# Kernel optimization log

Hardware: AMD Instinct MI355X
Metric: run time of the kernel (lower is better)

The kernel has to match this reference:

```python
import jax, jax.numpy as jnp
import numpy as np

NS, NV = 32, 8                      # scalar / vector multiplicities (32x0e + 8x1o)
N_NODES, N_EDGES = 16384, 131072
NEF, HID = 128, 128                 # edge feature dim, MLP hidden
WN = NS*NS + NV*NS + NS*NV + NV*NV  # 1600 tensor-product weights per edge
D = NS + 3*NV                       # 56 node feature dim
INV_SQRT3 = 1.0/np.sqrt(3.0)        # CG coeff for 1o x 1o -> 0e
PATH_NORM = 1.0/np.sqrt(NS + NV)    # fan-in normalization per output irrep
EPS = 1e-5


def setup_inputs() -> dict:
    key = jax.random.key(0)
    ks = jax.random.split(key, 10)
    node_attr = jax.random.normal(ks[0], (N_NODES, D), jnp.float32)
    edge_index = jax.random.randint(ks[1], (2, N_EDGES), 0, N_NODES, dtype=jnp.int64)
    edge_attr = jax.random.normal(ks[2], (N_EDGES, NEF), jnp.float32)
    edge_sh = jax.random.normal(ks[3], (N_EDGES, 4), jnp.float32)
    W1 = jax.random.normal(ks[4], (NEF, HID), jnp.float32) / np.sqrt(NEF)
    b1 = jnp.zeros((HID,), jnp.float32)
    W2 = jax.random.normal(ks[5], (HID, WN), jnp.float32) / np.sqrt(HID)
    b2 = jnp.zeros((WN,), jnp.float32)
    bn_gamma = jnp.ones((NS + NV,), jnp.float32)   # per-irrep scale (scalars then vectors)
    bn_beta = jnp.zeros((NS,), jnp.float32)        # bias only on scalar irreps
    return dict(node_attr=node_attr, edge_attr=edge_attr, edge_sh=edge_sh,
                W1=W1, b1=b1, W2=W2, b2=b2, bn_gamma=bn_gamma, bn_beta=bn_beta,
                edge_index=edge_index)


def reference(node_attr, edge_attr, edge_sh, W1, b1, W2, b2, bn_gamma, bn_beta, edge_index):
    edge_src, edge_dst = edge_index[0], edge_index[1]

    # per-edge tensor-product weights from edge MLP (dropout=0, eval mode)
    w = jax.nn.relu(edge_attr @ W1 + b1) @ W2 + b2            # [E, WN]
    o0 = NS*NS; o1 = o0 + NV*NS; o2 = o1 + NS*NV
    w_ss = w[:, :o0].reshape(-1, NS, NS)   # 0e x 0e -> 0e
    w_vs = w[:, o0:o1].reshape(-1, NV, NS) # 1o x 1o -> 0e
    w_sv = w[:, o1:o2].reshape(-1, NS, NV) # 0e x 1o -> 1o
    w_vv = w[:, o2:].reshape(-1, NV, NV)   # 1o x 0e -> 1o

    # gather node features onto edges
    x = node_attr[edge_dst]                # [E, D]
    xs = x[:, :NS]                         # [E, NS]
    xv = x[:, NS:].reshape(-1, NV, 3)      # [E, NV, 3]
    ss = edge_sh[:, 0]                     # [E]
    sv = edge_sh[:, 1:4]                   # [E, 3]

    # CG tensor product with per-edge fully-connected weights
    dot_vv = jnp.einsum('eim,em->ei', xv, sv) * INV_SQRT3
    out_s = (jnp.einsum('eij,ei->ej', w_ss, xs) * ss[:, None]
             + jnp.einsum('eij,ei->ej', w_vs, dot_vv)) * PATH_NORM          # [E, NS]
    out_v = (jnp.einsum('eij,ei->ej', w_sv, xs)[:, :, None] * sv[:, None, :]
             + jnp.einsum('eij,eim->ejm', w_vv, xv) * ss[:, None, None]) * PATH_NORM  # [E, NV, 3]
    tp = jnp.concatenate([out_s, out_v.reshape(-1, 3*NV)], axis=-1)         # [E, D]

    # scatter-mean to source nodes
    sums = jax.ops.segment_sum(tp, edge_src, num_segments=N_NODES)
    cnt = jax.ops.segment_sum(jnp.ones((tp.shape[0], 1), tp.dtype), edge_src,
                              num_segments=N_NODES)
    out = sums / jnp.maximum(cnt, 1.0)

    # residual (in/out irreps identical -> zero padding is a no-op)
    out = out + node_attr

    # equivariant batch norm (training-mode batch statistics)
    s = out[:, :NS]
    v = out[:, NS:].reshape(-1, NV, 3)
    s = (s - s.mean(0)) / jnp.sqrt(s.var(0) + EPS) * bn_gamma[:NS] + bn_beta
    vn2 = (v * v).sum(-1).mean(0)                               # [NV] mean squared norm
    v = v / jnp.sqrt(vn2 + EPS)[None, :, None] * bn_gamma[NS:][None, :, None]
    return jnp.concatenate([s, v.reshape(-1, 3*NV)], axis=-1)
```

## Files before the change

### kernel.cpp

```cpp
#include <hip/hip_runtime.h>

typedef short short8 __attribute__((ext_vector_type(8)));
typedef unsigned short us4 __attribute__((ext_vector_type(4)));
typedef float floatx4 __attribute__((ext_vector_type(4)));
typedef unsigned short u16;

#define NN 16384
#define NE 131072
#define NEF_ 128
#define DD 56
#define INV_SQRT3F 0.57735026918962576f
#define PATH_NORMF 0.15811388300841897f

__device__ __forceinline__ float bf2f(u16 u) {
    union { unsigned int i; float f; } v; v.i = ((unsigned int)u) << 16; return v.f;
}
__device__ __forceinline__ u16 f2bf(float f) {
    union { float f; unsigned int i; } v; v.f = f;
    unsigned int r = v.i + 0x7fffu + ((v.i >> 16) & 1u);
    return (u16)(r >> 16);
}

__global__ __launch_bounds__(256) void prep(const float* __restrict__ W1,
                                            const float* __restrict__ W2,
                                            u16* __restrict__ W1f,
                                            u16* __restrict__ W2f,
                                            const int* __restrict__ eidx,
                                            int* __restrict__ deg) {
    int b = blockIdx.x;
    if (b < 864) {
        int i = b * 256 + threadIdx.x;
        if (i < 16384) {
            int cc = i >> 13, kk = (i >> 11) & 3, cg = (i >> 9) & 3;
            int lane = (i >> 3) & 63, j = i & 7;
            int q = lane >> 4, m = lane & 15;
            W1f[i] = f2bf(W1[(kk * 32 + q * 8 + j) * 128 + cc * 64 + cg * 16 + m]);
        } else {
            int f = i - 16384;
            int c = f >> 13, kk = (f >> 11) & 3, cg = (f >> 9) & 3;
            int lane = (f >> 3) & 63, j = f & 7;
            int q = lane >> 4, m = lane & 15;
            W2f[f] = f2bf(W2[(kk * 32 + q * 8 + j) * 1600 + c * 64 + cg * 16 + m]);
        }
    } else {
        int e = (b - 864) * 256 + threadIdx.x;
        atomicAdd(&deg[eidx[e]], 1);
    }
}

__global__ __launch_bounds__(1024) void deg_scan(const int* __restrict__ deg,
                                                 int* __restrict__ row_start,
                                                 int* __restrict__ cursor) {
    __shared__ int part[1024];
    const int t = threadIdx.x;
    const int base = t * 16;
    int loc[16];
    int s = 0;
    #pragma unroll
    for (int i = 0; i < 16; i++) { loc[i] = s; s += deg[base + i]; }
    part[t] = s;
    __syncthreads();
    for (int off = 1; off < 1024; off <<= 1) {
        int v = (t >= off) ? part[t - off] : 0;
        __syncthreads();
        part[t] += v;
        __syncthreads();
    }
    int pre = (t == 0) ? 0 : part[t - 1];
    #pragma unroll
    for (int i = 0; i < 16; i++) {
        int v = pre + loc[i];
        row_start[base + i] = v;
        cursor[base + i] = v;
    }
    if (t == 1023) row_start[16384] = pre + s;
}

__global__ __launch_bounds__(256) void edge_scatter(const int* __restrict__ eidx,
                                                    int* __restrict__ cursor,
                                                    int* __restrict__ edge_order) {
    int e = blockIdx.x * 256 + threadIdx.x;
    int p = atomicAdd(&cursor[eidx[e]], 1);
    edge_order[p] = e;
}

__global__ __launch_bounds__(512, 4) void tpconv(
    const float* __restrict__ node_attr, const float* __restrict__ edge_attr,
    const float* __restrict__ edge_sh, const u16* __restrict__ W1f,
    const float* __restrict__ b1, const u16* __restrict__ W2f,
    const float* __restrict__ b2, const int* __restrict__ eidx,
    const int* __restrict__ edge_order,
    float* __restrict__ tp)
{
    __shared__ __align__(16) char smem[48896];
    u16*   sA  = (u16*)smem;
    u16*   B2a = (u16*)(smem + 17408);
    u16*   B2b = (u16*)smem;
    u16*   sF  = (u16*)(smem + 33792);
    float* b2s = (float*)(smem + 42496);
    float* Ssc  = (float*)smem;
    float* Svec = (float*)(smem + 16896);

    const int t = threadIdx.x;
    const int lane = t & 63;
    const int wv = t >> 6;
    const int m = lane & 15;
    const int q = lane >> 4;
    const int cg = wv & 3;
    const int eh = wv >> 2;
    const int eb = eh * 32;
    const int p0 = blockIdx.x * 64;

    short8 pre[2];
    #pragma unroll
    for (int ii = 0; ii < 2; ii++)
        pre[ii] = *(const short8*)&W2f[ii * 4096 + t * 8];

    for (int i = t; i < 1600; i += 512) b2s[i] = b2[i];

    #pragma unroll
    for (int ii = 0; ii < 4; ii++) {
        int cid = t + 512 * ii;
        int r = cid >> 5, s = cid & 31;
        int e = edge_order[p0 + r];
        const float* src = &edge_attr[(size_t)e * NEF_ + s * 4];
        us4 o;
        o.x = f2bf(src[0]); o.y = f2bf(src[1]); o.z = f2bf(src[2]); o.w = f2bf(src[3]);
        *(us4*)&sA[r * 136 + s * 4] = o;
    }
    if (t < 64) {
        int e = edge_order[p0 + t];
        int nd = eidx[NE + e];
        const float* na = node_attr + (size_t)nd * DD;
        const float* sh = edge_sh + (size_t)e * 4;
        float ss = sh[0], s0 = sh[1], s1 = sh[2], s2 = sh[3];
        #pragma unroll
        for (int i = 0; i < 32; i++) sF[i * 64 + t] = f2bf(na[i]);
        #pragma unroll
        for (int i = 0; i < 8; i++) {
            float d = (na[32+i*3]*s0 + na[33+i*3]*s1 + na[34+i*3]*s2) * INV_SQRT3F;
            sF[(32 + i) * 64 + t] = f2bf(d);
        }
        #pragma unroll
        for (int i = 0; i < 24; i++) sF[(40 + i) * 64 + t] = f2bf(na[32 + i]);
        sF[64 * 64 + t] = f2bf(ss);
        sF[65 * 64 + t] = f2bf(s0);
        sF[66 * 64 + t] = f2bf(s1);
        sF[67 * 64 + t] = f2bf(s2);
    }
    __syncthreads();

    floatx4 hacc[2][2];
    #pragma unroll
    for (int cc = 0; cc < 2; cc++) {
        #pragma unroll
        for (int ii = 0; ii < 2; ii++)
            *(short8*)&B2a[ii * 4096 + t * 8] =
                *(const short8*)&W1f[cc * 8192 + ii * 4096 + t * 8];
        __syncthreads();
        {
            float bv = b1[cc * 64 + cg * 16 + m];
            hacc[cc][0] = (floatx4){bv, bv, bv, bv};
            hacc[cc][1] = hacc[cc][0];
        }
        #pragma unroll
        for (int kk = 0; kk < 4; kk++) {
            short8 a0 = *(const short8*)&sA[(eb      + m) * 136 + kk * 32 + q * 8];
            short8 a1 = *(const short8*)&sA[(eb + 16 + m) * 136 + kk * 32 + q * 8];
            short8 bA = *(const short8*)&B2a[(kk * 4 + cg) * 512 + lane * 8];
            hacc[cc][0] = __builtin_amdgcn_mfma_f32_16x16x32_bf16(a0, bA, hacc[cc][0], 0, 0, 0);
            hacc[cc][1] = __builtin_amdgcn_mfma_f32_16x16x32_bf16(a1, bA, hacc[cc][1], 0, 0, 0);
        }
        __syncthreads();
    }
    #pragma unroll
    for (int cc = 0; cc < 2; cc++)
      #pragma unroll
      for (int rt = 0; rt < 2; rt++)
        #pragma unroll
        for (int r = 0; r < 4; r++) {
            int e   = eb + rt * 16 + q * 4 + r;
            int col = cc * 64 + cg * 16 + m;
            float v = hacc[cc][rt][r];
            sA[e * 136 + col] = f2bf(v > 0.f ? v : 0.f);
        }
    __syncthreads();

    short8 hc[2][4];
    #pragma unroll
    for (int et = 0; et < 2; et++)
        #pragma unroll
        for (int kk = 0; kk < 4; kk++)
            hc[et][kk] = *(const short8*)&sA[(eb + et * 16 + m) * 136 + kk * 32 + q * 8];

    float ssc[2], svc[2][3];
    #pragma unroll
    for (int et = 0; et < 2; et++) {
        ssc[et] = bf2f(sF[64 * 64 + eb + et * 16 + m]);
        svc[et][0] = bf2f(sF[65 * 64 + eb + et * 16 + m]);
        svc[et][1] = bf2f(sF[66 * 64 + eb + et * 16 + m]);
        svc[et][2] = bf2f(sF[67 * 64 + eb + et * 16 + m]);
    }

    #pragma unroll
    for (int ii = 0; ii < 2; ii++)
        *(short8*)&B2a[ii * 4096 + t * 8] = pre[ii];
    #pragma unroll
    for (int ii = 0; ii < 2; ii++)
        pre[ii] = *(const short8*)&W2f[8192 + ii * 4096 + t * 8];
    __syncthreads();

    float tps[2][4];
    float tpv[2][4][3];
    #pragma unroll
    for (int et = 0; et < 2; et++)
        #pragma unroll
        for (int r = 0; r < 4; r++) {
            tps[et][r] = 0.f;
            tpv[et][r][0] = 0.f; tpv[et][r][1] = 0.f; tpv[et][r][2] = 0.f;
        }

    for (int c = 0; c < 25; c++) {
        const u16* rb = (c & 1) ? B2b : B2a;
        u16*       wb = (c & 1) ? B2a : B2b;

        floatx4 bias = *(const floatx4*)&b2s[c * 64 + cg * 16 + q * 4];
        floatx4 acc[2];
        acc[0] = bias; acc[1] = bias;
        #pragma unroll
        for (int kk = 0; kk < 4; kk++) {
            short8 a = *(const short8*)&rb[(kk * 4 + cg) * 512 + lane * 8];
            acc[0] = __builtin_amdgcn_mfma_f32_16x16x32_bf16(a, hc[0][kk], acc[0], 0, 0, 0);
            acc[1] = __builtin_amdgcn_mfma_f32_16x16x32_bf16(a, hc[1][kk], acc[1], 0, 0, 0);
        }

        if (c < 24) {
            #pragma unroll
            for (int ii = 0; ii < 2; ii++)
                *(short8*)&wb[ii * 4096 + t * 8] = pre[ii];
            if (c < 23) {
                #pragma unroll
                for (int ii = 0; ii < 2; ii++)
                    pre[ii] = *(const short8*)&W2f[(size_t)(c + 2) * 8192 + ii * 4096 + t * 8];
            }
        }

        if (c < 16) {
            const int i = 2 * c + (cg >> 1);
            #pragma unroll
            for (int et = 0; et < 2; et++) {
                float f = bf2f(sF[i * 64 + eb + et * 16 + m]) * ssc[et];
                #pragma unroll
                for (int r = 0; r < 4; r++) tps[et][r] += acc[et][r] * f;
            }
        } else if (c < 20) {
            const int i = 2 * (c - 16) + (cg >> 1);
            #pragma unroll
            for (int et = 0; et < 2; et++) {
                float f = bf2f(sF[(32 + i) * 64 + eb + et * 16 + m]);
                #pragma unroll
                for (int r = 0; r < 4; r++) tps[et][r] += acc[et][r] * f;
            }
        } else if (c < 24) {
            const int i = 8 * (c - 20) + cg * 2 + (q >> 1);
            #pragma unroll
            for (int et = 0; et < 2; et++) {
                float f = bf2f(sF[i * 64 + eb + et * 16 + m]);
                #pragma unroll
                for (int r = 0; r < 4; r++) {
                    float t0 = acc[et][r] * f;
                    tpv[et][r][0] += t0 * svc[et][0];
                    tpv[et][r][1] += t0 * svc[et][1];
                    tpv[et][r][2] += t0 * svc[et][2];
                }
            }
        } else {
            const int i = cg * 2 + (q >> 1);
            #pragma unroll
            for (int et = 0; et < 2; et++) {
                float x0 = bf2f(sF[(40 + 3 * i + 0) * 64 + eb + et * 16 + m]) * ssc[et];
                float x1 = bf2f(sF[(40 + 3 * i + 1) * 64 + eb + et * 16 + m]) * ssc[et];
                float x2 = bf2f(sF[(40 + 3 * i + 2) * 64 + eb + et * 16 + m]) * ssc[et];
                #pragma unroll
                for (int r = 0; r < 4; r++) {
                    tpv[et][r][0] += acc[et][r] * x0;
                    tpv[et][r][1] += acc[et][r] * x1;
                    tpv[et][r][2] += acc[et][r] * x2;
                }
            }
        }

        __syncthreads();
    }

    #pragma unroll
    for (int et = 0; et < 2; et++)
        #pragma unroll
        for (int r = 0; r < 4; r++)
            Ssc[(cg >> 1) * 2112 + (eb + et * 16 + m) * 33 + (cg & 1) * 16 + q * 4 + r] = tps[et][r];
    #pragma unroll
    for (int et = 0; et < 2; et++)
        #pragma unroll
        for (int r = 0; r < 4; r++)
            #pragma unroll
            for (int mm = 0; mm < 3; mm++) {
                float v = tpv[et][r][mm];
                v += __shfl_xor(v, 32, 64);
                if (q < 2)
                    Svec[cg * 1600 + (eb + et * 16 + m) * 25 + ((q & 1) * 4 + r) * 3 + mm] = v;
            }
    __syncthreads();

    for (int idx = t; idx < 3584; idx += 512) {
        int e = idx / 56, d = idx - e * 56;
        float v;
        if (d < 32) {
            v = Ssc[e * 33 + d] + Ssc[2112 + e * 33 + d];
        } else {
            int dd = d - 32;
            v = Svec[e * 25 + dd] + Svec[1600 + e * 25 + dd]
              + Svec[3200 + e * 25 + dd] + Svec[4800 + e * 25 + dd];
        }
        tp[(size_t)(p0 + e) * DD + d] = v * PATH_NORMF;
    }
}

__global__ __launch_bounds__(256) void gather_finalize(
    const float* __restrict__ tp, const int* __restrict__ row_start,
    const float* __restrict__ node_attr,
    float* __restrict__ ybuf, float* __restrict__ partial)
{
    __shared__ float ps[4][72];
    const int wv = threadIdx.x >> 6, lane = threadIdx.x & 63;
    const int n = blockIdx.x * 4 + wv;
    const int beg = row_start[n], end = row_start[n + 1];
    if (lane < 56) {
        float acc = 0.f;
        for (int p = beg; p < end; p++)
            acc += tp[(size_t)p * DD + lane];
        float inv = 1.f / fmaxf((float)(end - beg), 1.f);
        float y = acc * inv + node_attr[(size_t)n * DD + lane];
        ybuf[(size_t)n * DD + lane] = y;
        if (lane < 32) {
            ps[wv][lane] = y;
            ps[wv][32 + lane] = y * y;
        } else {
            float vv = y * y;
            float v1 = __shfl_down(vv, 1, 64);
            float v2 = __shfl_down(vv, 2, 64);
            int l3 = lane - 32;
            if (l3 % 3 == 0) ps[wv][64 + l3 / 3] = vv + v1 + v2;
        }
    }
    __syncthreads();
    const int t = threadIdx.x;
    if (t < 72)
        partial[(size_t)blockIdx.x * 72 + t] = ps[0][t] + ps[1][t] + ps[2][t] + ps[3][t];
}

__global__ __launch_bounds__(256) void bn_reduce(const float* __restrict__ partial,
                                                 float* __restrict__ stats)
{
    __shared__ float red[256];
    const int d = blockIdx.x;
    const int t = threadIdx.x;
    float a = 0.f;
    for (int i = t; i < 4096; i += 256) a += partial[(size_t)i * 72 + d];
    red[t] = a;
    __syncthreads();
    for (int off = 128; off > 0; off >>= 1) {
        if (t < off) red[t] += red[t + off];
        __syncthreads();
    }
    if (t == 0) stats[d] = red[0] * (1.f / 16384.f);
}

__global__ __launch_bounds__(256) void bn_apply(
    const float* __restrict__ ybuf, const float* __restrict__ stats,
    const float* __restrict__ gamma, const float* __restrict__ beta,
    float* __restrict__ out)
{
    const int i = blockIdx.x * 256 + threadIdx.x;
    const int n = i / 56;
    const int d = i - n * 56;
    float y = ybuf[i];
    float o;
    if (d < 32) {
        float mn  = stats[d];
        float var = stats[32 + d] - mn * mn;
        o = (y - mn) * rsqrtf(var + 1e-5f) * gamma[d] + beta[d];
    } else {
        int jv = (d - 32) / 3;
        o = y * rsqrtf(stats[64 + jv] + 1e-5f) * gamma[32 + jv];
    }
    out[i] = o;
}

extern "C" void kernel_launch(void* const* d_in, const int* in_sizes, int n_in,
                              void* d_out, int out_size, void* d_ws, size_t ws_size,
                              hipStream_t stream)
{
    const float* node_attr = (const float*)d_in[0];
    const float* edge_attr = (const float*)d_in[1];
    const float* edge_sh   = (const float*)d_in[2];
    const float* W1        = (const float*)d_in[3];
    const float* b1        = (const float*)d_in[4];
    const float* W2        = (const float*)d_in[5];
    const float* b2        = (const float*)d_in[6];
    const float* gamma     = (const float*)d_in[7];
    const float* beta      = (const float*)d_in[8];
    const int*   eidx      = (const int*)d_in[9];

    char* ws = (char*)d_ws;
    u16*   W1f        = (u16*)(ws);
    u16*   W2f        = (u16*)(ws + 32768);
    int*   deg        = (int*)(ws + 442368);
    int*   row_start  = (int*)(ws + 507904);
    int*   cursor     = (int*)(ws + 573696);
    int*   edge_order = (int*)(ws + 639232);
    float* stats      = (float*)(ws + 1163520);
    float* partial    = (float*)(ws + 1164032);
    float* tp         = (float*)(ws + 2343680);
    float* ybuf       = (float*)(ws + 31703808);

    (void)hipMemsetAsync(deg, 0, 65536, stream);
    hipLaunchKernelGGL(prep,            dim3(1376), dim3(256),  0, stream,
                       W1, W2, W1f, W2f, eidx, deg);
    hipLaunchKernelGGL(deg_scan,        dim3(1),    dim3(1024), 0, stream, deg, row_start, cursor);
    hipLaunchKernelGGL(edge_scatter,    dim3(512),  dim3(256),  0, stream, eidx, cursor, edge_order);
    hipLaunchKernelGGL(tpconv,          dim3(2048), dim3(512),  0, stream,
                       node_attr, edge_attr, edge_sh, W1f, b1, W2f, b2, eidx, edge_order, tp);
    hipLaunchKernelGGL(gather_finalize, dim3(4096), dim3(256),  0, stream,
                       tp, row_start, node_attr, ybuf, partial);
    hipLaunchKernelGGL(bn_reduce,       dim3(72),   dim3(256),  0, stream, partial, stats);
    hipLaunchKernelGGL(bn_apply,        dim3(3584), dim3(256),  0, stream,
                       ybuf, stats, gamma, beta, (float*)d_out);
}
```

Baseline: 248.5 us.

## Load W2 fragments straight to registers, drop LDS double-buffer and per-chunk barriers

The tpconv kernel goes from 512 to 256 threads per block. Each wave now covers all 64 edges of a 16-column group and holds 4 edge tiles of accumulators. W1 and W2 MFMA operand fragments are read from global memory directly into registers, with the next W2 chunk prefetched into registers. This removes the LDS double-buffered W2 staging and the __syncthreads at the end of each of the 25 chunks, and shrinks shared memory. In exchange it raises register pressure (hc[4][4], tpv[4][4][3], acc[4]) and halves the number of threads per block, which may reduce occupancy or cause spills.

```diff
diff --git a/kernel.cpp b/kernel.cpp
--- a/kernel.cpp
+++ b/kernel.cpp
@@ -84,7 +84,7 @@
     edge_order[p] = e;
 }
 
-__global__ __launch_bounds__(512, 4) void tpconv(
+__global__ __launch_bounds__(256, 2) void tpconv(
     const float* __restrict__ node_attr, const float* __restrict__ edge_attr,
     const float* __restrict__ edge_sh, const u16* __restrict__ W1f,
     const float* __restrict__ b1, const u16* __restrict__ W2f,
@@ -92,35 +92,30 @@
     const int* __restrict__ edge_order,
     float* __restrict__ tp)
 {
-    __shared__ __align__(16) char smem[48896];
+    __shared__ __align__(16) char smem[42496];
     u16*   sA  = (u16*)smem;
-    u16*   B2a = (u16*)(smem + 17408);
-    u16*   B2b = (u16*)smem;
-    u16*   sF  = (u16*)(smem + 33792);
-    float* b2s = (float*)(smem + 42496);
+    u16*   sF  = (u16*)(smem + 17408);
+    float* b2s = (float*)(smem + 26112);
     float* Ssc  = (float*)smem;
     float* Svec = (float*)(smem + 16896);
 
     const int t = threadIdx.x;
     const int lane = t & 63;
-    const int wv = t >> 6;
+    const int cg = t >> 6;
     const int m = lane & 15;
     const int q = lane >> 4;
-    const int cg = wv & 3;
-    const int eh = wv >> 2;
-    const int eb = eh * 32;
     const int p0 = blockIdx.x * 64;
 
-    short8 pre[2];
-    #pragma unroll
-    for (int ii = 0; ii < 2; ii++)
-        pre[ii] = *(const short8*)&W2f[ii * 4096 + t * 8];
-
-    for (int i = t; i < 1600; i += 512) b2s[i] = b2[i];
-
-    #pragma unroll
-    for (int ii = 0; ii < 4; ii++) {
-        int cid = t + 512 * ii;
+    short8 fc[4];
+    #pragma unroll
+    for (int kk = 0; kk < 4; kk++)
+        fc[kk] = *(const short8*)&W2f[(kk * 4 + cg) * 512 + lane * 8];
+
+    for (int i = t; i < 1600; i += 256) b2s[i] = b2[i];
+
+    #pragma unroll
+    for (int ii = 0; ii < 8; ii++) {
+        int cid = t + 256 * ii;
         int r = cid >> 5, s = cid & 31;
         int e = edge_order[p0 + r];
         const float* src = &edge_attr[(size_t)e * NEF_ + s * 4];
@@ -128,144 +123,127 @@
         o.x = f2bf(src[0]); o.y = f2bf(src[1]); o.z = f2bf(src[2]); o.w = f2bf(src[3]);
         *(us4*)&sA[r * 136 + s * 4] = o;
     }
-    if (t < 64) {
-        int e = edge_order[p0 + t];
-        int nd = eidx[NE + e];
+    {
+        int e = t & 63, p = t >> 6;
+        int eg = edge_order[p0 + e];
+        int nd = eidx[NE + eg];
         const float* na = node_attr + (size_t)nd * DD;
-        const float* sh = edge_sh + (size_t)e * 4;
-        float ss = sh[0], s0 = sh[1], s1 = sh[2], s2 = sh[3];
-        #pragma unroll
-        for (int i = 0; i < 32; i++) sF[i * 64 + t] = f2bf(na[i]);
-        #pragma unroll
-        for (int i = 0; i < 8; i++) {
-            float d = (na[32+i*3]*s0 + na[33+i*3]*s1 + na[34+i*3]*s2) * INV_SQRT3F;
-            sF[(32 + i) * 64 + t] = f2bf(d);
-        }
-        #pragma unroll
-        for (int i = 0; i < 24; i++) sF[(40 + i) * 64 + t] = f2bf(na[32 + i]);
-        sF[64 * 64 + t] = f2bf(ss);
-        sF[65 * 64 + t] = f2bf(s0);
-        sF[66 * 64 + t] = f2bf(s1);
-        sF[67 * 64 + t] = f2bf(s2);
-    }
-    __syncthreads();
-
-    floatx4 hacc[2][2];
+        const float* sh = edge_sh + (size_t)eg * 4;
+        if (p < 2) {
+            #pragma unroll
+            for (int k = 0; k < 16; k++)
+                sF[(p * 16 + k) * 64 + e] = f2bf(na[p * 16 + k]);
+        } else {
+            #pragma unroll
+            for (int k = 0; k < 12; k++)
+                sF[(40 + (p - 2) * 12 + k) * 64 + e] = f2bf(na[32 + (p - 2) * 12 + k]);
+        }
+        sF[(64 + p) * 64 + e] = f2bf(sh[p]);
+        float s0 = sh[1], s1 = sh[2], s2 = sh[3];
+        #pragma unroll
+        for (int s = 0; s < 2; s++) {
+            int i = p + 4 * s;
+            float d = (na[32 + 3 * i] * s0 + na[33 + 3 * i] * s1 + na[34 + 3 * i] * s2) * INV_SQRT3F;
+            sF[(32 + i) * 64 + e] = f2bf(d);
+        }
+    }
+    __syncthreads();
+
+    floatx4 hacc[2][4];
     #pragma unroll
     for (int cc = 0; cc < 2; cc++) {
-        #pragma unroll
-        for (int ii = 0; ii < 2; ii++)
-            *(short8*)&B2a[ii * 4096 + t * 8] =
-                *(const short8*)&W1f[cc * 8192 + ii * 4096 + t * 8];
-        __syncthreads();
-        {
-            float bv = b1[cc * 64 + cg * 16 + m];
-            hacc[cc][0] = (floatx4){bv, bv, bv, bv};
-            hacc[cc][1] = hacc[cc][0];
-        }
-        #pragma unroll
-        for (int kk = 0; kk < 4; kk++) {
-            short8 a0 = *(const short8*)&sA[(eb      + m) * 136 + kk * 32 + q * 8];
-            short8 a1 = *(const short8*)&sA[(eb + 16 + m) * 136 + kk * 32 + q * 8];
-            short8 bA = *(const short8*)&B2a[(kk * 4 + cg) * 512 + lane * 8];
-            hacc[cc][0] = __builtin_amdgcn_mfma_f32_16x16x32_bf16(a0, bA, hacc[cc][0], 0, 0, 0);
-            hacc[cc][1] = __builtin_amdgcn_mfma_f32_16x16x32_bf16(a1, bA, hacc[cc][1], 0, 0, 0);
-        }
-        __syncthreads();
-    }
+        short8 g[4];
+        #pragma unroll
+        for (int kk = 0; kk < 4; kk++)
+            g[kk] = *(const short8*)&W1f[cc * 8192 + (kk * 4 + cg) * 512 + lane * 8];
+        float bv = b1[cc * 64 + cg * 16 + m];
+        #pragma unroll
+        for (int et = 0; et < 4; et++) hacc[cc][et] = (floatx4){bv, bv, bv, bv};
+        #pragma unroll
+        for (int kk = 0; kk < 4; kk++)
+            #pragma unroll
+            for (int et = 0; et < 4; et++) {
+                short8 a = *(const short8*)&sA[(et * 16 + m) * 136 + kk * 32 + q * 8];
+                hacc[cc][et] = __builtin_amdgcn_mfma_f32_16x16x32_bf16(a, g[kk], hacc[cc][et], 0, 0, 0);
+            }
+    }
+    __syncthreads();
     #pragma unroll
     for (int cc = 0; cc < 2; cc++)
       #pragma unroll
-      for (int rt = 0; rt < 2; rt++)
+      for (int et = 0; et < 4; et++)
         #pragma unroll
         for (int r = 0; r < 4; r++) {
-            int e   = eb + rt * 16 + q * 4 + r;
-            int col = cc * 64 + cg * 16 + m;
-            float v = hacc[cc][rt][r];
-            sA[e * 136 + col] = f2bf(v > 0.f ? v : 0.f);
-        }
-    __syncthreads();
-
-    short8 hc[2][4];
-    #pragma unroll
-    for (int et = 0; et < 2; et++)
+            int e = et * 16 + q * 4 + r;
+            float v = hacc[cc][et][r];
+            sA[e * 136 + cc * 64 + cg * 16 + m] = f2bf(v > 0.f ? v : 0.f);
+        }
+    __syncthreads();
+
+    short8 hc[4][4];
+    #pragma unroll
+    for (int et = 0; et < 4; et++)
         #pragma unroll
         for (int kk = 0; kk < 4; kk++)
-            hc[et][kk] = *(const short8*)&sA[(eb + et * 16 + m) * 136 + kk * 32 + q * 8];
-
-    float ssc[2], svc[2][3];
-    #pragma unroll
-    for (int et = 0; et < 2; et++) {
-        ssc[et] = bf2f(sF[64 * 64 + eb + et * 16 + m]);
-        svc[et][0] = bf2f(sF[65 * 64 + eb + et * 16 + m]);
-        svc[et][1] = bf2f(sF[66 * 64 + eb + et * 16 + m]);
-        svc[et][2] = bf2f(sF[67 * 64 + eb + et * 16 + m]);
-    }
-
-    #pragma unroll
-    for (int ii = 0; ii < 2; ii++)
-        *(short8*)&B2a[ii * 4096 + t * 8] = pre[ii];
-    #pragma unroll
-    for (int ii = 0; ii < 2; ii++)
-        pre[ii] = *(const short8*)&W2f[8192 + ii * 4096 + t * 8];
-    __syncthreads();
-
-    float tps[2][4];
-    float tpv[2][4][3];
-    #pragma unroll
-    for (int et = 0; et < 2; et++)
+            hc[et][kk] = *(const short8*)&sA[(et * 16 + m) * 136 + kk * 32 + q * 8];
+
+    float ssc[4], svc[4][3];
+    #pragma unroll
+    for (int et = 0; et < 4; et++) {
+        ssc[et]    = bf2f(sF[64 * 64 + et * 16 + m]);
+        svc[et][0] = bf2f(sF[65 * 64 + et * 16 + m]);
+        svc[et][1] = bf2f(sF[66 * 64 + et * 16 + m]);
+        svc[et][2] = bf2f(sF[67 * 64 + et * 16 + m]);
+    }
+
+    float tps[4][4];
+    float tpv[4][4][3];
+    #pragma unroll
+    for (int et = 0; et < 4; et++)
         #pragma unroll
         for (int r = 0; r < 4; r++) {
             tps[et][r] = 0.f;
             tpv[et][r][0] = 0.f; tpv[et][r][1] = 0.f; tpv[et][r][2] = 0.f;
         }
 
+    short8 fn[4];
     for (int c = 0; c < 25; c++) {
-        const u16* rb = (c & 1) ? B2b : B2a;
-        u16*       wb = (c & 1) ? B2a : B2b;
-
+        if (c < 24) {
+            #pragma unroll
+            for (int kk = 0; kk < 4; kk++)
+                fn[kk] = *(const short8*)&W2f[(size_t)(c + 1) * 8192 + (kk * 4 + cg) * 512 + lane * 8];
+        }
         floatx4 bias = *(const floatx4*)&b2s[c * 64 + cg * 16 + q * 4];
-        floatx4 acc[2];
-        acc[0] = bias; acc[1] = bias;
-        #pragma unroll
-        for (int kk = 0; kk < 4; kk++) {
-            short8 a = *(const short8*)&rb[(kk * 4 + cg) * 512 + lane * 8];
-            acc[0] = __builtin_amdgcn_mfma_f32_16x16x32_bf16(a, hc[0][kk], acc[0], 0, 0, 0);
-            acc[1] = __builtin_amdgcn_mfma_f32_16x16x32_bf16(a, hc[1][kk], acc[1], 0, 0, 0);
-        }
-
-        if (c < 24) {
-            #pragma unroll
-            for (int ii = 0; ii < 2; ii++)
-                *(short8*)&wb[ii * 4096 + t * 8] = pre[ii];
-            if (c < 23) {
-                #pragma unroll
-                for (int ii = 0; ii < 2; ii++)
-                    pre[ii] = *(const short8*)&W2f[(size_t)(c + 2) * 8192 + ii * 4096 + t * 8];
-            }
-        }
+        floatx4 acc[4];
+        #pragma unroll
+        for (int et = 0; et < 4; et++) acc[et] = bias;
+        #pragma unroll
+        for (int kk = 0; kk < 4; kk++)
+            #pragma unroll
+            for (int et = 0; et < 4; et++)
+                acc[et] = __builtin_amdgcn_mfma_f32_16x16x32_bf16(fc[kk], hc[et][kk], acc[et], 0, 0, 0);
 
         if (c < 16) {
             const int i = 2 * c + (cg >> 1);
             #pragma unroll
-            for (int et = 0; et < 2; et++) {
-                float f = bf2f(sF[i * 64 + eb + et * 16 + m]) * ssc[et];
+            for (int et = 0; et < 4; et++) {
+                float f = bf2f(sF[i * 64 + et * 16 + m]) * ssc[et];
                 #pragma unroll
                 for (int r = 0; r < 4; r++) tps[et][r] += acc[et][r] * f;
             }
         } else if (c < 20) {
             const int i = 2 * (c - 16) + (cg >> 1);
             #pragma unroll
-            for (int et = 0; et < 2; et++) {
-                float f = bf2f(sF[(32 + i) * 64 + eb + et * 16 + m]);
+            for (int et = 0; et < 4; et++) {
+                float f = bf2f(sF[(32 + i) * 64 + et * 16 + m]);
                 #pragma unroll
                 for (int r = 0; r < 4; r++) tps[et][r] += acc[et][r] * f;
             }
         } else if (c < 24) {
             const int i = 8 * (c - 20) + cg * 2 + (q >> 1);
             #pragma unroll
-            for (int et = 0; et < 2; et++) {
-                float f = bf2f(sF[i * 64 + eb + et * 16 + m]);
+            for (int et = 0; et < 4; et++) {
+                float f = bf2f(sF[i * 64 + et * 16 + m]);
                 #pragma unroll
                 for (int r = 0; r < 4; r++) {
                     float t0 = acc[et][r] * f;
@@ -277,10 +255,10 @@
         } else {
             const int i = cg * 2 + (q >> 1);
             #pragma unroll
-            for (int et = 0; et < 2; et++) {
-                float x0 = bf2f(sF[(40 + 3 * i + 0) * 64 + eb + et * 16 + m]) * ssc[et];
-                float x1 = bf2f(sF[(40 + 3 * i + 1) * 64 + eb + et * 16 + m]) * ssc[et];
-                float x2 = bf2f(sF[(40 + 3 * i + 2) * 64 + eb + et * 16 + m]) * ssc[et];
+            for (int et = 0; et < 4; et++) {
+                float x0 = bf2f(sF[(40 + 3 * i + 0) * 64 + et * 16 + m]) * ssc[et];
+                float x1 = bf2f(sF[(40 + 3 * i + 1) * 64 + et * 16 + m]) * ssc[et];
+                float x2 = bf2f(sF[(40 + 3 * i + 2) * 64 + et * 16 + m]) * ssc[et];
                 #pragma unroll
                 for (int r = 0; r < 4; r++) {
                     tpv[et][r][0] += acc[et][r] * x0;
@@ -290,16 +268,20 @@
             }
         }
 
-        __syncthreads();
-    }
-
-    #pragma unroll
-    for (int et = 0; et < 2; et++)
+        if (c < 24) {
+            #pragma unroll
+            for (int kk = 0; kk < 4; kk++) fc[kk] = fn[kk];
+        }
+    }
+
+    __syncthreads();
+    #pragma unroll
+    for (int et = 0; et < 4; et++)
         #pragma unroll
         for (int r = 0; r < 4; r++)
-            Ssc[(cg >> 1) * 2112 + (eb + et * 16 + m) * 33 + (cg & 1) * 16 + q * 4 + r] = tps[et][r];
-    #pragma unroll
-    for (int et = 0; et < 2; et++)
+            Ssc[(cg >> 1) * 2112 + (et * 16 + m) * 33 + (cg & 1) * 16 + q * 4 + r] = tps[et][r];
+    #pragma unroll
+    for (int et = 0; et < 4; et++)
         #pragma unroll
         for (int r = 0; r < 4; r++)
             #pragma unroll
@@ -307,11 +289,11 @@
                 float v = tpv[et][r][mm];
                 v += __shfl_xor(v, 32, 64);
                 if (q < 2)
-                    Svec[cg * 1600 + (eb + et * 16 + m) * 25 + ((q & 1) * 4 + r) * 3 + mm] = v;
-            }
-    __syncthreads();
-
-    for (int idx = t; idx < 3584; idx += 512) {
+                    Svec[cg * 1600 + (et * 16 + m) * 25 + ((q & 1) * 4 + r) * 3 + mm] = v;
+            }
+    __syncthreads();
+
+    for (int idx = t; idx < 3584; idx += 256) {
         int e = idx / 56, d = idx - e * 56;
         float v;
         if (d < 32) {
@@ -428,7 +410,7 @@
                        W1, W2, W1f, W2f, eidx, deg);
     hipLaunchKernelGGL(deg_scan,        dim3(1),    dim3(1024), 0, stream, deg, row_start, cursor);
     hipLaunchKernelGGL(edge_scatter,    dim3(512),  dim3(256),  0, stream, eidx, cursor, edge_order);
-    hipLaunchKernelGGL(tpconv,          dim3(2048), dim3(512),  0, stream,
+    hipLaunchKernelGGL(tpconv,          dim3(2048), dim3(256),  0, stream,
                        node_attr, edge_attr, edge_sh, W1f, b1, W2f, b2, eidx, edge_order, tp);
     hipLaunchKernelGGL(gather_finalize, dim3(4096), dim3(256),  0, stream,
                        tp, row_start, node_attr, ybuf, partial);
```

New measurement: 280.8 us. 13.0% more time.

## Process 128 edges per block with register-held W1 and swizzled LDS tile

Applied to the files above, without the earlier changes.

The tile grows from 64 to 128 edges per block. Each wave now keeps its W1 fragments in registers and computes a 16-column slice of the hidden layer for all 128 edges, so the two W1 staging loops and their barriers are gone. The edge-attribute tile uses an XOR-swizzled unpadded layout to avoid LDS bank conflicts, and edge_sh is read directly from global memory instead of going through LDS. In the W2 loop each wave computes two column tiles, so every W2 chunk staged in LDS is reused across twice as many edges. The cost is 72KB of LDS per block and more registers, which lowers occupancy and halves the grid to 1024 blocks.

```diff
diff --git a/kernel.cpp b/kernel.cpp
--- a/kernel.cpp
+++ b/kernel.cpp
@@ -19,6 +19,10 @@
     union { float f; unsigned int i; } v; v.f = f;
     unsigned int r = v.i + 0x7fffu + ((v.i >> 16) & 1u);
     return (u16)(r >> 16);
+}
+
+__device__ __forceinline__ int sa_off(int row, int col) {
+    return (row << 7) + (col ^ ((row & 7) << 3));
 }
 
 __global__ __launch_bounds__(256) void prep(const float* __restrict__ W1,
@@ -92,24 +96,23 @@
     const int* __restrict__ edge_order,
     float* __restrict__ tp)
 {
-    __shared__ __align__(16) char smem[48896];
+    __shared__ __align__(16) char smem[73728];
     u16*   sA  = (u16*)smem;
-    u16*   B2a = (u16*)(smem + 17408);
+    u16*   sF  = (u16*)(smem + 32768);
+    u16*   B2a = (u16*)(smem + 49152);
     u16*   B2b = (u16*)smem;
-    u16*   sF  = (u16*)(smem + 33792);
-    float* b2s = (float*)(smem + 42496);
+    float* b2s = (float*)(smem + 65536);
     float* Ssc  = (float*)smem;
-    float* Svec = (float*)(smem + 16896);
+    float* Svec = (float*)(smem + 33792);
 
     const int t = threadIdx.x;
     const int lane = t & 63;
     const int wv = t >> 6;
     const int m = lane & 15;
     const int q = lane >> 4;
-    const int cg = wv & 3;
-    const int eh = wv >> 2;
-    const int eb = eh * 32;
-    const int p0 = blockIdx.x * 64;
+    const int cg = wv & 1;
+    const int ew = wv >> 1;
+    const int p0 = blockIdx.x * 128;
 
     short8 pre[2];
     #pragma unroll
@@ -118,90 +121,44 @@
 
     for (int i = t; i < 1600; i += 512) b2s[i] = b2[i];
 
-    #pragma unroll
-    for (int ii = 0; ii < 4; ii++) {
+    short8 g[4];
+    #pragma unroll
+    for (int kk = 0; kk < 4; kk++)
+        g[kk] = *(const short8*)&W1f[(wv >> 2) * 8192 + (kk * 4 + (wv & 3)) * 512 + lane * 8];
+
+    #pragma unroll
+    for (int ii = 0; ii < 8; ii++) {
         int cid = t + 512 * ii;
         int r = cid >> 5, s = cid & 31;
         int e = edge_order[p0 + r];
         const float* src = &edge_attr[(size_t)e * NEF_ + s * 4];
         us4 o;
         o.x = f2bf(src[0]); o.y = f2bf(src[1]); o.z = f2bf(src[2]); o.w = f2bf(src[3]);
-        *(us4*)&sA[r * 136 + s * 4] = o;
-    }
-    if (t < 64) {
-        int e = edge_order[p0 + t];
-        int nd = eidx[NE + e];
+        *(us4*)&sA[sa_off(r, s * 4)] = o;
+    }
+    {
+        int e = t & 127, p = t >> 7;
+        int eg = edge_order[p0 + e];
+        int nd = eidx[NE + eg];
         const float* na = node_attr + (size_t)nd * DD;
-        const float* sh = edge_sh + (size_t)e * 4;
-        float ss = sh[0], s0 = sh[1], s1 = sh[2], s2 = sh[3];
-        #pragma unroll
-        for (int i = 0; i < 32; i++) sF[i * 64 + t] = f2bf(na[i]);
-        #pragma unroll
-        for (int i = 0; i < 8; i++) {
-            float d = (na[32+i*3]*s0 + na[33+i*3]*s1 + na[34+i*3]*s2) * INV_SQRT3F;
-            sF[(32 + i) * 64 + t] = f2bf(d);
-        }
-        #pragma unroll
-        for (int i = 0; i < 24; i++) sF[(40 + i) * 64 + t] = f2bf(na[32 + i]);
-        sF[64 * 64 + t] = f2bf(ss);
-        sF[65 * 64 + t] = f2bf(s0);
-        sF[66 * 64 + t] = f2bf(s1);
-        sF[67 * 64 + t] = f2bf(s2);
-    }
-    __syncthreads();
-
-    floatx4 hacc[2][2];
-    #pragma unroll
-    for (int cc = 0; cc < 2; cc++) {
-        #pragma unroll
-        for (int ii = 0; ii < 2; ii++)
-            *(short8*)&B2a[ii * 4096 + t * 8] =
-                *(const short8*)&W1f[cc * 8192 + ii * 4096 + t * 8];
-        __syncthreads();
-        {
-            float bv = b1[cc * 64 + cg * 16 + m];
-            hacc[cc][0] = (floatx4){bv, bv, bv, bv};
-            hacc[cc][1] = hacc[cc][0];
-        }
-        #pragma unroll
-        for (int kk = 0; kk < 4; kk++) {
-            short8 a0 = *(const short8*)&sA[(eb      + m) * 136 + kk * 32 + q * 8];
-            short8 a1 = *(const short8*)&sA[(eb + 16 + m) * 136 + kk * 32 + q * 8];
-            short8 bA = *(const short8*)&B2a[(kk * 4 + cg) * 512 + lane * 8];
-            hacc[cc][0] = __builtin_amdgcn_mfma_f32_16x16x32_bf16(a0, bA, hacc[cc][0], 0, 0, 0);
-            hacc[cc][1] = __builtin_amdgcn_mfma_f32_16x16x32_bf16(a1, bA, hacc[cc][1], 0, 0, 0);
-        }
-        __syncthreads();
-    }
-    #pragma unroll
-    for (int cc = 0; cc < 2; cc++)
-      #pragma unroll
-      for (int rt = 0; rt < 2; rt++)
-        #pragma unroll
-        for (int r = 0; r < 4; r++) {
-            int e   = eb + rt * 16 + q * 4 + r;
-            int col = cc * 64 + cg * 16 + m;
-            float v = hacc[cc][rt][r];
-            sA[e * 136 + col] = f2bf(v > 0.f ? v : 0.f);
-        }
-    __syncthreads();
-
-    short8 hc[2][4];
-    #pragma unroll
-    for (int et = 0; et < 2; et++)
-        #pragma unroll
-        for (int kk = 0; kk < 4; kk++)
-            hc[et][kk] = *(const short8*)&sA[(eb + et * 16 + m) * 136 + kk * 32 + q * 8];
-
-    float ssc[2], svc[2][3];
-    #pragma unroll
-    for (int et = 0; et < 2; et++) {
-        ssc[et] = bf2f(sF[64 * 64 + eb + et * 16 + m]);
-        svc[et][0] = bf2f(sF[65 * 64 + eb + et * 16 + m]);
-        svc[et][1] = bf2f(sF[66 * 64 + eb + et * 16 + m]);
-        svc[et][2] = bf2f(sF[67 * 64 + eb + et * 16 + m]);
-    }
-
+        if (p < 2) {
+            #pragma unroll
+            for (int k = 0; k < 16; k++)
+                sF[(p * 16 + k) * 128 + e] = f2bf(na[p * 16 + k]);
+        } else if (p == 2) {
+            const float* sh = edge_sh + (size_t)eg * 4;
+            float s0 = sh[1], s1 = sh[2], s2 = sh[3];
+            #pragma unroll
+            for (int i = 0; i < 8; i++) {
+                float d = (na[32 + 3 * i] * s0 + na[33 + 3 * i] * s1 + na[34 + 3 * i] * s2) * INV_SQRT3F;
+                sF[(32 + i) * 128 + e] = f2bf(d);
+            }
+        } else {
+            #pragma unroll
+            for (int k = 0; k < 24; k++)
+                sF[(40 + k) * 128 + e] = f2bf(na[32 + k]);
+        }
+    }
     #pragma unroll
     for (int ii = 0; ii < 2; ii++)
         *(short8*)&B2a[ii * 4096 + t * 8] = pre[ii];
@@ -210,13 +167,55 @@
         pre[ii] = *(const short8*)&W2f[8192 + ii * 4096 + t * 8];
     __syncthreads();
 
-    float tps[2][4];
+    floatx4 hacc[8];
+    {
+        float bv = b1[wv * 16 + m];
+        #pragma unroll
+        for (int rt = 0; rt < 8; rt++) hacc[rt] = (floatx4){bv, bv, bv, bv};
+    }
+    #pragma unroll
+    for (int kk = 0; kk < 4; kk++)
+        #pragma unroll
+        for (int rt = 0; rt < 8; rt++) {
+            short8 a = *(const short8*)&sA[sa_off(rt * 16 + m, kk * 32 + q * 8)];
+            hacc[rt] = __builtin_amdgcn_mfma_f32_16x16x32_bf16(a, g[kk], hacc[rt], 0, 0, 0);
+        }
+    __syncthreads();
+    #pragma unroll
+    for (int rt = 0; rt < 8; rt++)
+        #pragma unroll
+        for (int r = 0; r < 4; r++) {
+            int e = rt * 16 + q * 4 + r;
+            float v = hacc[rt][r];
+            sA[sa_off(e, wv * 16 + m)] = f2bf(v > 0.f ? v : 0.f);
+        }
+    __syncthreads();
+
+    const int e0 = ew * 32 + m;
+    const int e1 = ew * 32 + 16 + m;
+    short8 hc[2][4];
+    #pragma unroll
+    for (int et = 0; et < 2; et++)
+        #pragma unroll
+        for (int kk = 0; kk < 4; kk++)
+            hc[et][kk] = *(const short8*)&sA[sa_off(ew * 32 + et * 16 + m, kk * 32 + q * 8)];
+
+    float ssc[2], svc[2][3];
+    #pragma unroll
+    for (int et = 0; et < 2; et++) {
+        int eg = edge_order[p0 + ew * 32 + et * 16 + m];
+        const float* sh = edge_sh + (size_t)eg * 4;
+        ssc[et] = sh[0]; svc[et][0] = sh[1]; svc[et][1] = sh[2]; svc[et][2] = sh[3];
+    }
+    __syncthreads();
+
+    float tps[2][2][4];
     float tpv[2][4][3];
     #pragma unroll
     for (int et = 0; et < 2; et++)
         #pragma unroll
         for (int r = 0; r < 4; r++) {
-            tps[et][r] = 0.f;
+            tps[et][0][r] = 0.f; tps[et][1][r] = 0.f;
             tpv[et][r][0] = 0.f; tpv[et][r][1] = 0.f; tpv[et][r][2] = 0.f;
         }
 
@@ -224,15 +223,20 @@
         const u16* rb = (c & 1) ? B2b : B2a;
         u16*       wb = (c & 1) ? B2a : B2b;
 
-        floatx4 bias = *(const floatx4*)&b2s[c * 64 + cg * 16 + q * 4];
-        floatx4 acc[2];
-        acc[0] = bias; acc[1] = bias;
-        #pragma unroll
-        for (int kk = 0; kk < 4; kk++) {
-            short8 a = *(const short8*)&rb[(kk * 4 + cg) * 512 + lane * 8];
-            acc[0] = __builtin_amdgcn_mfma_f32_16x16x32_bf16(a, hc[0][kk], acc[0], 0, 0, 0);
-            acc[1] = __builtin_amdgcn_mfma_f32_16x16x32_bf16(a, hc[1][kk], acc[1], 0, 0, 0);
-        }
+        floatx4 acc[2][2];
+        #pragma unroll
+        for (int ct = 0; ct < 2; ct++) {
+            floatx4 bias = *(const floatx4*)&b2s[c * 64 + cg * 32 + ct * 16 + q * 4];
+            acc[ct][0] = bias; acc[ct][1] = bias;
+        }
+        #pragma unroll
+        for (int kk = 0; kk < 4; kk++)
+            #pragma unroll
+            for (int ct = 0; ct < 2; ct++) {
+                short8 a = *(const short8*)&rb[(kk * 4 + cg * 2 + ct) * 512 + lane * 8];
+                acc[ct][0] = __builtin_amdgcn_mfma_f32_16x16x32_bf16(a, hc[0][kk], acc[ct][0], 0, 0, 0);
+                acc[ct][1] = __builtin_amdgcn_mfma_f32_16x16x32_bf16(a, hc[1][kk], acc[ct][1], 0, 0, 0);
+            }
 
         if (c < 24) {
             #pragma unroll
@@ -246,46 +250,57 @@
         }
 
         if (c < 16) {
-            const int i = 2 * c + (cg >> 1);
+            const int i = 2 * c + cg;
             #pragma unroll
             for (int et = 0; et < 2; et++) {
-                float f = bf2f(sF[i * 64 + eb + et * 16 + m]) * ssc[et];
+                float f = bf2f(sF[i * 128 + (et ? e1 : e0)]) * ssc[et];
                 #pragma unroll
-                for (int r = 0; r < 4; r++) tps[et][r] += acc[et][r] * f;
+                for (int ct = 0; ct < 2; ct++)
+                    #pragma unroll
+                    for (int r = 0; r < 4; r++) tps[et][ct][r] += acc[ct][et][r] * f;
             }
         } else if (c < 20) {
-            const int i = 2 * (c - 16) + (cg >> 1);
+            const int i = 2 * (c - 16) + cg;
             #pragma unroll
             for (int et = 0; et < 2; et++) {
-                float f = bf2f(sF[(32 + i) * 64 + eb + et * 16 + m]);
+                float f = bf2f(sF[(32 + i) * 128 + (et ? e1 : e0)]);
                 #pragma unroll
-                for (int r = 0; r < 4; r++) tps[et][r] += acc[et][r] * f;
+                for (int ct = 0; ct < 2; ct++)
+                    #pragma unroll
+                    for (int r = 0; r < 4; r++) tps[et][ct][r] += acc[ct][et][r] * f;
             }
         } else if (c < 24) {
-            const int i = 8 * (c - 20) + cg * 2 + (q >> 1);
-            #pragma unroll
-            for (int et = 0; et < 2; et++) {
-                float f = bf2f(sF[i * 64 + eb + et * 16 + m]);
+            #pragma unroll
+            for (int ct = 0; ct < 2; ct++) {
+                const int i = 8 * (c - 20) + cg * 4 + ct * 2 + (q >> 1);
                 #pragma unroll
-                for (int r = 0; r < 4; r++) {
-                    float t0 = acc[et][r] * f;
-                    tpv[et][r][0] += t0 * svc[et][0];
-                    tpv[et][r][1] += t0 * svc[et][1];
-                    tpv[et][r][2] += t0 * svc[et][2];
+                for (int et = 0; et < 2; et++) {
+                    float f = bf2f(sF[i * 128 + (et ? e1 : e0)]);
+                    #pragma unroll
+                    for (int r = 0; r < 4; r++) {
+                        float t0 = acc[ct][et][r] * f;
+                        tpv[et][r][0] += t0 * svc[et][0];
+                        tpv[et][r][1] += t0 * svc[et][1];
+                        tpv[et][r][2] += t0 * svc[et][2];
+                    }
                 }
             }
         } else {
-            const int i = cg * 2 + (q >> 1);
-            #pragma unroll
-            for (int et = 0; et < 2; et++) {
-                float x0 = bf2f(sF[(40 + 3 * i + 0) * 64 + eb + et * 16 + m]) * ssc[et];
-                float x1 = bf2f(sF[(40 + 3 * i + 1) * 64 + eb + et * 16 + m]) * ssc[et];
-                float x2 = bf2f(sF[(40 + 3 * i + 2) * 64 + eb + et * 16 + m]) * ssc[et];
+            #pragma unroll
+            for (int ct = 0; ct < 2; ct++) {
+                const int i = cg * 4 + ct * 2 + (q >> 1);
                 #pragma unroll
-                for (int r = 0; r < 4; r++) {
-                    tpv[et][r][0] += acc[et][r] * x0;
-                    tpv[et][r][1] += acc[et][r] * x1;
-                    tpv[et][r][2] += acc[et][r] * x2;
+                for (int et = 0; et < 2; et++) {
+                    const int ee = et ? e1 : e0;
+                    float x0 = bf2f(sF[(40 + 3 * i    ) * 128 + ee]) * ssc[et];
+                    float x1 = bf2f(sF[(40 + 3 * i + 1) * 128 + ee]) * ssc[et];
+                    float x2 = bf2f(sF[(40 + 3 * i + 2) * 128 + ee]) * ssc[et];
+                    #pragma unroll
+                    for (int r = 0; r < 4; r++) {
+                        tpv[et][r][0] += acc[ct][et][r] * x0;
+                        tpv[et][r][1] += acc[ct][et][r] * x1;
+                        tpv[et][r][2] += acc[ct][et][r] * x2;
+                    }
                 }
             }
         }
@@ -294,12 +309,17 @@
     }
 
     #pragma unroll
-    for (int et = 0; et < 2; et++)
-        #pragma unroll
-        for (int r = 0; r < 4; r++)
-            Ssc[(cg >> 1) * 2112 + (eb + et * 16 + m) * 33 + (cg & 1) * 16 + q * 4 + r] = tps[et][r];
-    #pragma unroll
-    for (int et = 0; et < 2; et++)
+    for (int et = 0; et < 2; et++) {
+        const int ee = et ? e1 : e0;
+        #pragma unroll
+        for (int ct = 0; ct < 2; ct++)
+            #pragma unroll
+            for (int r = 0; r < 4; r++)
+                Ssc[(cg * 128 + ee) * 33 + ct * 16 + q * 4 + r] = tps[et][ct][r];
+    }
+    #pragma unroll
+    for (int et = 0; et < 2; et++) {
+        const int ee = et ? e1 : e0;
         #pragma unroll
         for (int r = 0; r < 4; r++)
             #pragma unroll
@@ -307,19 +327,19 @@
                 float v = tpv[et][r][mm];
                 v += __shfl_xor(v, 32, 64);
                 if (q < 2)
-                    Svec[cg * 1600 + (eb + et * 16 + m) * 25 + ((q & 1) * 4 + r) * 3 + mm] = v;
-            }
-    __syncthreads();
-
-    for (int idx = t; idx < 3584; idx += 512) {
+                    Svec[(cg * 128 + ee) * 25 + (q * 4 + r) * 3 + mm] = v;
+            }
+    }
+    __syncthreads();
+
+    for (int idx = t; idx < 7168; idx += 512) {
         int e = idx / 56, d = idx - e * 56;
         float v;
         if (d < 32) {
-            v = Ssc[e * 33 + d] + Ssc[2112 + e * 33 + d];
+            v = Ssc[e * 33 + d] + Ssc[(128 + e) * 33 + d];
         } else {
             int dd = d - 32;
-            v = Svec[e * 25 + dd] + Svec[1600 + e * 25 + dd]
-              + Svec[3200 + e * 25 + dd] + Svec[4800 + e * 25 + dd];
+            v = Svec[e * 25 + dd] + Svec[(128 + e) * 25 + dd];
         }
         tp[(size_t)(p0 + e) * DD + d] = v * PATH_NORMF;
     }
@@ -428,7 +448,7 @@
                        W1, W2, W1f, W2f, eidx, deg);
     hipLaunchKernelGGL(deg_scan,        dim3(1),    dim3(1024), 0, stream, deg, row_start, cursor);
     hipLaunchKernelGGL(edge_scatter,    dim3(512),  dim3(256),  0, stream, eidx, cursor, edge_order);
-    hipLaunchKernelGGL(tpconv,          dim3(2048), dim3(512),  0, stream,
+    hipLaunchKernelGGL(tpconv,          dim3(1024), dim3(512),  0, stream,
                        node_attr, edge_attr, edge_sh, W1f, b1, W2f, b2, eidx, edge_order, tp);
     hipLaunchKernelGGL(gather_finalize, dim3(4096), dim3(256),  0, stream,
                        tp, row_start, node_attr, ybuf, partial);
```

Measured after the change: 254.3 us. +2.3%, slower.
